# Optimization experiments

Measured on AMD Instinct MI355X. Metric: run time of the kernel, lower is better.

The kernel has to match this reference:

```python
import jax, jax.numpy as jnp
import numpy as np

N_NODES = 100000


def _lightgcn_layer(x, src, dst, norm):
    # message: norm * x[src]; aggregate: mean over incoming edges at dst
    msg = norm[:, None] * x[src]                                   # [E+N, D]
    s = jax.ops.segment_sum(msg, dst, num_segments=N_NODES)        # [N, D]
    cnt = jax.ops.segment_sum(jnp.ones_like(norm), dst, num_segments=N_NODES)
    return s / cnt[:, None]                                        # deg>=1 due to self-loops


def _graph_embeddings(emb, edge_index):
    n = emb.shape[0]
    loop = jnp.arange(n, dtype=edge_index.dtype)
    src = jnp.concatenate([edge_index[0], loop])                   # self-loops appended
    dst = jnp.concatenate([edge_index[1], loop])
    deg = jax.ops.segment_sum(jnp.ones(src.shape[0], emb.dtype), src, num_segments=N_NODES)
    dis = deg ** -0.5
    norm = dis[src] * dis[dst]
    x = emb
    acc = emb
    for _ in range(2):  # num_layers
        x = _lightgcn_layer(x, src, dst, norm)
        acc = acc + x
    return acc / 3.0  # mean over (num_layers + 1) embeddings


def setup_inputs() -> dict:
    key = jax.random.key(0)
    k1, k2, k3, k4 = jax.random.split(key, 4)
    emb = jax.random.normal(k1, (N_NODES, 128), dtype=jnp.float32) * 0.02
    edge_index = jax.random.randint(k2, (2, 600000), 0, N_NODES, dtype=jnp.int64)
    items = jax.random.randint(k3, (4096, 1), 0, N_NODES, dtype=jnp.int64)
    samples = jax.random.randint(k4, (4096, 100), 0, N_NODES, dtype=jnp.int64)
    return {"emb": emb, "edge_index": edge_index, "items": items, "samples": samples}


def reference(emb, edge_index, items, samples):
    embeddings = _graph_embeddings(emb, edge_index)                # [N, D]
    item_emb = embeddings[items]                                   # [B, 1, D]
    sample_emb = embeddings[samples]                               # [B, S, D]
    scores = jnp.einsum('bod,bsd->bos', item_emb, sample_emb)      # [B, 1, S]
    return scores.squeeze(1)                                       # [B, S]
```

## Files before the change

### kernel.cpp

```cpp
#include <hip/hip_runtime.h>

#define NN 100000
#define D 128
#define W 32
#define EPT 2
#define HRS 50000
#define HWORDS 25000
#define HSPLIT 64

__device__ __forceinline__ unsigned short f2bf(float f) {
    unsigned u = __float_as_uint(f);
    u += 0x7FFF + ((u >> 16) & 1);
    return (unsigned short)(u >> 16);
}
__device__ __forceinline__ float bflo(unsigned u) { return __uint_as_float(u << 16); }
__device__ __forceinline__ float bfhi(unsigned u) { return __uint_as_float(u & 0xFFFF0000u); }
__device__ __forceinline__ unsigned pack2(float a, float b) {
    return (unsigned)f2bf(a) | ((unsigned)f2bf(b) << 16);
}
__device__ __forceinline__ void addrow(float* acc, const uint4 v, float w) {
    acc[0] += w * bflo(v.x); acc[1] += w * bfhi(v.x);
    acc[2] += w * bflo(v.y); acc[3] += w * bfhi(v.y);
    acc[4] += w * bflo(v.z); acc[5] += w * bfhi(v.z);
    acc[6] += w * bflo(v.w); acc[7] += w * bfhi(v.w);
}

__global__ __launch_bounds__(256) void hist1_kernel(const int* __restrict__ src,
                                                    unsigned* __restrict__ part,
                                                    int* __restrict__ fillc, int E) {
    __shared__ unsigned h[HWORDS];
    {
        const int per = (NN + 2 * HSPLIT - 1) / (2 * HSPLIT);
        int z0 = blockIdx.x * per;
        int z1 = min(z0 + per, NN);
        for (int t = z0 + (int)threadIdx.x; t < z1; t += 256) fillc[t] = 0;
    }
    int r = blockIdx.x >> 6, c = blockIdx.x & (HSPLIT - 1);
    for (int t = threadIdx.x; t < HWORDS; t += 256) h[t] = 0;
    __syncthreads();
    int chunk = (E + HSPLIT - 1) / HSPLIT;
    int e0 = c * chunk, e1 = min(e0 + chunk, E);
    int lo = r * HRS;
    for (int e = e0 + (int)threadIdx.x; e < e1; e += 256) {
        unsigned s = (unsigned)(src[e] - lo);
        if (s < (unsigned)HRS) atomicAdd(&h[s >> 1], 1u << ((s & 1u) << 4));
    }
    __syncthreads();
    unsigned* dstp = part + (size_t)c * (2 * HWORDS) + (size_t)r * HWORDS;
    for (int t = threadIdx.x; t < HWORDS; t += 256) dstp[t] = h[t];
}

__global__ __launch_bounds__(256) void histB_kernel(const unsigned* __restrict__ part,
                                                    int* __restrict__ deg, int nw) {
    int w = blockIdx.x * 256 + threadIdx.x;
    if (w >= nw) return;
    unsigned s = 0;
    #pragma unroll
    for (int c = 0; c < HSPLIT; ++c) s += part[(size_t)c * (2 * HWORDS) + w];
    deg[2 * w] = (int)(s & 0xFFFFu);
    deg[2 * w + 1] = (int)(s >> 16);
}

__global__ __launch_bounds__(256) void hetero_kernel(const int* __restrict__ src,
                                                     const int* __restrict__ dst,
                                                     const float* __restrict__ emb,
                                                     int* __restrict__ fillc,
                                                     int* __restrict__ ell,
                                                     unsigned short* __restrict__ y0h,
                                                     int E, int EB, int total, int total8) {
    int b = blockIdx.x;
    int lo = (int)(((long long)b * EB) / total);
    int hi = (int)(((long long)(b + 1) * EB) / total);
    if (hi > lo) {
        int e0 = lo * (256 * EPT) + threadIdx.x;
        int e1 = e0 + 256;
        int sa = -1, sb = -1, da = 0, db = 0;
        if (e0 < E) { sa = src[e0]; da = dst[e0]; }
        if (e1 < E) { sb = src[e1]; db = dst[e1]; }
        int pa = -1, pb = -1;
        if (sa >= 0) pa = atomicAdd(&fillc[da], 1);
        if (sb >= 0) pb = atomicAdd(&fillc[db], 1);
        if (sa >= 0 && pa < W) ell[(size_t)da * W + pa] = sa;
        if (sb >= 0 && pb < W) ell[(size_t)db * W + pb] = sb;
    } else {
        int t = (b - hi) * 256 + threadIdx.x;
        if (t < total8) {
            const float4 a = ((const float4*)emb)[t * 2];
            const float4 c = ((const float4*)emb)[t * 2 + 1];
            uint4 o;
            o.x = pack2(a.x, a.y);
            o.y = pack2(a.z, a.w);
            o.z = pack2(c.x, c.y);
            o.w = pack2(c.z, c.w);
            ((uint4*)y0h)[t] = o;
        }
    }
}

__global__ __launch_bounds__(256) void gather1_kernel(const int* __restrict__ ell,
                                                      const int* __restrict__ fillc,
                                                      const int* __restrict__ deg,
                                                      const unsigned short* __restrict__ y0h,
                                                      unsigned short* __restrict__ y1h, int n) {
    unsigned t = blockIdx.x * 256u + threadIdx.x;
    unsigned i = t >> 4, q = t & 15u;
    if (i >= (unsigned)n) return;
    int len = fillc[i];
    int lenc = len > W ? W : len;
    const int* base = ell + (size_t)i * W;
    float wd = rsqrtf((float)deg[i] + 1.0f);
    const uint4 ph = *(const uint4*)(y0h + (size_t)i * D + q * 8);
    float acc[8] = {0.f, 0.f, 0.f, 0.f, 0.f, 0.f, 0.f, 0.f};
    addrow(acc, ph, wd);
    int j = 0;
    for (; j + 4 <= lenc; j += 4) {
        const int4 ss = *(const int4*)(base + j);
        float w0 = rsqrtf((float)deg[ss.x] + 1.0f);
        float w1 = rsqrtf((float)deg[ss.y] + 1.0f);
        float w2 = rsqrtf((float)deg[ss.z] + 1.0f);
        float w3 = rsqrtf((float)deg[ss.w] + 1.0f);
        const uint4 v0 = *(const uint4*)(y0h + (size_t)ss.x * D + q * 8);
        const uint4 v1 = *(const uint4*)(y0h + (size_t)ss.y * D + q * 8);
        const uint4 v2 = *(const uint4*)(y0h + (size_t)ss.z * D + q * 8);
        const uint4 v3 = *(const uint4*)(y0h + (size_t)ss.w * D + q * 8);
        addrow(acc, v0, w0);
        addrow(acc, v1, w1);
        addrow(acc, v2, w2);
        addrow(acc, v3, w3);
    }
    for (; j < lenc; ++j) {
        int s0 = base[j];
        float w0 = rsqrtf((float)deg[s0] + 1.0f);
        const uint4 v0 = *(const uint4*)(y0h + (size_t)s0 * D + q * 8);
        addrow(acc, v0, w0);
    }
    float ci = 1.0f / (float)(len + 1);
    float f1 = ci * wd * wd;
    uint4 o;
    o.x = pack2(f1 * acc[0], f1 * acc[1]);
    o.y = pack2(f1 * acc[2], f1 * acc[3]);
    o.z = pack2(f1 * acc[4], f1 * acc[5]);
    o.w = pack2(f1 * acc[6], f1 * acc[7]);
    *(uint4*)(y1h + (size_t)i * D + q * 8) = o;
}

__global__ __launch_bounds__(256) void gather2_kernel(const int* __restrict__ ell,
                                                      const int* __restrict__ fillc,
                                                      const int* __restrict__ deg,
                                                      const unsigned short* __restrict__ y1h,
                                                      const unsigned short* __restrict__ y0h,
                                                      unsigned short* __restrict__ finh, int n) {
    unsigned t = blockIdx.x * 256u + threadIdx.x;
    unsigned i = t >> 4, q = t & 15u;
    if (i >= (unsigned)n) return;
    int len = fillc[i];
    int lenc = len > W ? W : len;
    const int* base = ell + (size_t)i * W;
    const uint4 ph = *(const uint4*)(y1h + (size_t)i * D + q * 8);
    const uint4 pe = *(const uint4*)(y0h + (size_t)i * D + q * 8);
    float self[8];
    self[0] = bflo(ph.x); self[1] = bfhi(ph.x);
    self[2] = bflo(ph.y); self[3] = bfhi(ph.y);
    self[4] = bflo(ph.z); self[5] = bfhi(ph.z);
    self[6] = bflo(ph.w); self[7] = bfhi(ph.w);
    float acc[8];
    #pragma unroll
    for (int k = 0; k < 8; ++k) acc[k] = self[k];
    int j = 0;
    for (; j + 4 <= lenc; j += 4) {
        const int4 ss = *(const int4*)(base + j);
        const uint4 v0 = *(const uint4*)(y1h + (size_t)ss.x * D + q * 8);
        const uint4 v1 = *(const uint4*)(y1h + (size_t)ss.y * D + q * 8);
        const uint4 v2 = *(const uint4*)(y1h + (size_t)ss.z * D + q * 8);
        const uint4 v3 = *(const uint4*)(y1h + (size_t)ss.w * D + q * 8);
        addrow(acc, v0, 1.0f);
        addrow(acc, v1, 1.0f);
        addrow(acc, v2, 1.0f);
        addrow(acc, v3, 1.0f);
    }
    for (; j < lenc; ++j) {
        int s0 = base[j];
        const uint4 v0 = *(const uint4*)(y1h + (size_t)s0 * D + q * 8);
        addrow(acc, v0, 1.0f);
    }
    float dp1 = (float)deg[i] + 1.0f;
    float wd = rsqrtf(dp1);
    float wdi = sqrtf(dp1);
    float ci = 1.0f / (float)(len + 1);
    float g = ci * wd;
    const float k3 = 1.0f / 3.0f;
    float e[8];
    e[0] = bflo(pe.x); e[1] = bfhi(pe.x);
    e[2] = bflo(pe.y); e[3] = bfhi(pe.y);
    e[4] = bflo(pe.z); e[5] = bfhi(pe.z);
    e[6] = bflo(pe.w); e[7] = bfhi(pe.w);
    float r[8];
    #pragma unroll
    for (int k = 0; k < 8; ++k) r[k] = (e[k] + self[k] * wdi + g * acc[k]) * k3;
    uint4 o;
    o.x = pack2(r[0], r[1]);
    o.y = pack2(r[2], r[3]);
    o.z = pack2(r[4], r[5]);
    o.w = pack2(r[6], r[7]);
    *(uint4*)(finh + (size_t)i * D + q * 8) = o;
}

__global__ __launch_bounds__(256) void scores_kernel(const unsigned short* __restrict__ finh,
                                                     const int* __restrict__ items,
                                                     const int* __restrict__ samples,
                                                     float* __restrict__ out, int S) {
    __shared__ float it[D];
    int b = blockIdx.x;
    if (threadIdx.x < 64) {
        unsigned u = ((const unsigned*)(finh + (size_t)items[b] * D))[threadIdx.x];
        it[threadIdx.x * 2] = bflo(u);
        it[threadIdx.x * 2 + 1] = bfhi(u);
    }
    __syncthreads();
    int g = threadIdx.x >> 4, lane = threadIdx.x & 15;
    float w[8];
    #pragma unroll
    for (int k = 0; k < 8; ++k) w[k] = it[lane * 8 + k];
    int s = g;
    for (; s + 16 < S; s += 32) {
        int node0 = samples[b * S + s];
        int node1 = samples[b * S + s + 16];
        const uint4 v0 = *(const uint4*)(finh + (size_t)node0 * D + lane * 8);
        const uint4 v1 = *(const uint4*)(finh + (size_t)node1 * D + lane * 8);
        float a0 = w[0] * bflo(v0.x) + w[1] * bfhi(v0.x) + w[2] * bflo(v0.y) + w[3] * bfhi(v0.y)
                 + w[4] * bflo(v0.z) + w[5] * bfhi(v0.z) + w[6] * bflo(v0.w) + w[7] * bfhi(v0.w);
        float a1 = w[0] * bflo(v1.x) + w[1] * bfhi(v1.x) + w[2] * bflo(v1.y) + w[3] * bfhi(v1.y)
                 + w[4] * bflo(v1.z) + w[5] * bfhi(v1.z) + w[6] * bflo(v1.w) + w[7] * bfhi(v1.w);
        #pragma unroll
        for (int o = 8; o; o >>= 1) {
            a0 += __shfl_xor(a0, o);
            a1 += __shfl_xor(a1, o);
        }
        if (lane == 0) {
            out[b * S + s] = a0;
            out[b * S + s + 16] = a1;
        }
    }
    if (s < S) {
        int node = samples[b * S + s];
        const uint4 v = *(const uint4*)(finh + (size_t)node * D + lane * 8);
        float a = w[0] * bflo(v.x) + w[1] * bfhi(v.x) + w[2] * bflo(v.y) + w[3] * bfhi(v.y)
                + w[4] * bflo(v.z) + w[5] * bfhi(v.z) + w[6] * bflo(v.w) + w[7] * bfhi(v.w);
        #pragma unroll
        for (int o = 8; o; o >>= 1) a += __shfl_xor(a, o);
        if (lane == 0) out[b * S + s] = a;
    }
}

extern "C" void kernel_launch(void* const* d_in, const int* in_sizes, int n_in,
                              void* d_out, int out_size, void* d_ws, size_t ws_size,
                              hipStream_t stream) {
    const float* emb = (const float*)d_in[0];
    const int* ei = (const int*)d_in[1];
    const int* items = (const int*)d_in[2];
    const int* samples = (const int*)d_in[3];
    float* out = (float*)d_out;

    const int E = in_sizes[1] / 2;
    const int B = in_sizes[2];
    const int S = in_sizes[3] / B;
    const int* src = ei;
    const int* dst = ei + E;

    int* deg = (int*)d_ws;
    int* fillc = deg + NN;
    int* ell = fillc + NN;
    unsigned* part = (unsigned*)(ell + (size_t)NN * W);
    unsigned short* y0h = (unsigned short*)(part + (size_t)HSPLIT * 2 * HWORDS);
    unsigned short* y1h = y0h + (size_t)NN * D;
    unsigned short* finh = y1h + (size_t)NN * D;

    hist1_kernel<<<2 * HSPLIT, 256, 0, stream>>>(src, part, fillc, E);

    const int EB = (E + 256 * EPT - 1) / (256 * EPT);
    const int total8 = NN * D / 8;
    const int CB = (total8 + 255) / 256;
    const int total = EB + CB;
    hetero_kernel<<<total, 256, 0, stream>>>(src, dst, emb, fillc, ell, y0h,
                                             E, EB, total, total8);

    histB_kernel<<<(2 * HWORDS + 255) / 256, 256, 0, stream>>>(part, deg, 2 * HWORDS);

    const int gblocks = (NN * 16 + 255) / 256;
    gather1_kernel<<<gblocks, 256, 0, stream>>>(ell, fillc, deg, y0h, y1h, NN);
    gather2_kernel<<<gblocks, 256, 0, stream>>>(ell, fillc, deg, y1h, y0h, finh, NN);

    scores_kernel<<<B, 256, 0, stream>>>(finh, items, samples, out, S);
}
```

Baseline: 146.4 us.

## Sort nodes by in-degree bucket to balance gather wavefronts

Adds a three-kernel counting sort (per-block histogram, single-block scan, scatter) that builds a permutation of nodes grouped by clamped neighbor count. Both gather kernels then process nodes in this permuted order so lanes in a wavefront have similar loop trip counts, reducing divergence and tail imbalance. This costs three extra small launches and an indirection through perm, and it breaks the contiguous node ordering of the self-row loads and output writes.

```diff
diff --git a/kernel.cpp b/kernel.cpp
--- a/kernel.cpp
+++ b/kernel.cpp
@@ -7,6 +7,11 @@
 #define HRS 50000
 #define HWORDS 25000
 #define HSPLIT 64
+#define LB 98
+#define NPB 1024
+#define NBINS 33
+#define SCTOT (NBINS * LB)
+#define SCPER 13
 
 __device__ __forceinline__ unsigned short f2bf(float f) {
     unsigned u = __float_as_uint(f);
@@ -97,14 +102,79 @@
     }
 }
 
+__global__ __launch_bounds__(256) void lenhistA_kernel(const int* __restrict__ fillc,
+                                                       int* __restrict__ bcnt, int n) {
+    __shared__ int h[NBINS];
+    int b = blockIdx.x;
+    if (threadIdx.x < NBINS) h[threadIdx.x] = 0;
+    __syncthreads();
+    int i0 = b * NPB, i1 = min(i0 + NPB, n);
+    for (int i = i0 + (int)threadIdx.x; i < i1; i += 256) {
+        int len = fillc[i]; if (len > 32) len = 32;
+        atomicAdd(&h[len], 1);
+    }
+    __syncthreads();
+    if (threadIdx.x < NBINS) bcnt[threadIdx.x * LB + b] = h[threadIdx.x];
+}
+
+__global__ __launch_bounds__(256) void lenscan_kernel(const int* __restrict__ bcnt,
+                                                      int* __restrict__ boff) {
+    __shared__ int ws[4];
+    int t = threadIdx.x;
+    int loc[SCPER];
+    int s = 0;
+    int base = t * SCPER;
+    #pragma unroll
+    for (int k = 0; k < SCPER; ++k) {
+        int idx = base + k;
+        int v = (idx < SCTOT) ? bcnt[idx] : 0;
+        loc[k] = s;
+        s += v;
+    }
+    int lane = t & 63, w = t >> 6;
+    int v = s;
+    #pragma unroll
+    for (int o = 1; o < 64; o <<= 1) { int y = __shfl_up(v, o); if (lane >= o) v += y; }
+    if (lane == 63) ws[w] = v;
+    __syncthreads();
+    int add = 0;
+    for (int k = 0; k < w; ++k) add += ws[k];
+    int excl = v + add - s;
+    #pragma unroll
+    for (int k = 0; k < SCPER; ++k) {
+        int idx = base + k;
+        if (idx < SCTOT) boff[idx] = excl + loc[k];
+    }
+}
+
+__global__ __launch_bounds__(256) void lenscat_kernel(const int* __restrict__ fillc,
+                                                      const int* __restrict__ boff,
+                                                      int* __restrict__ perm, int n) {
+    __shared__ int basev[NBINS], cnt[NBINS];
+    int b = blockIdx.x;
+    if (threadIdx.x < NBINS) {
+        basev[threadIdx.x] = boff[threadIdx.x * LB + b];
+        cnt[threadIdx.x] = 0;
+    }
+    __syncthreads();
+    int i0 = b * NPB, i1 = min(i0 + NPB, n);
+    for (int i = i0 + (int)threadIdx.x; i < i1; i += 256) {
+        int len = fillc[i]; if (len > 32) len = 32;
+        int r = atomicAdd(&cnt[len], 1);
+        perm[basev[len] + r] = i;
+    }
+}
+
 __global__ __launch_bounds__(256) void gather1_kernel(const int* __restrict__ ell,
                                                       const int* __restrict__ fillc,
                                                       const int* __restrict__ deg,
+                                                      const int* __restrict__ perm,
                                                       const unsigned short* __restrict__ y0h,
                                                       unsigned short* __restrict__ y1h, int n) {
     unsigned t = blockIdx.x * 256u + threadIdx.x;
-    unsigned i = t >> 4, q = t & 15u;
-    if (i >= (unsigned)n) return;
+    unsigned g = t >> 4, q = t & 15u;
+    if (g >= (unsigned)n) return;
+    unsigned i = (unsigned)perm[g];
     int len = fillc[i];
     int lenc = len > W ? W : len;
     const int* base = ell + (size_t)i * W;
@@ -147,12 +217,14 @@
 __global__ __launch_bounds__(256) void gather2_kernel(const int* __restrict__ ell,
                                                       const int* __restrict__ fillc,
                                                       const int* __restrict__ deg,
+                                                      const int* __restrict__ perm,
                                                       const unsigned short* __restrict__ y1h,
                                                       const unsigned short* __restrict__ y0h,
                                                       unsigned short* __restrict__ finh, int n) {
     unsigned t = blockIdx.x * 256u + threadIdx.x;
-    unsigned i = t >> 4, q = t & 15u;
-    if (i >= (unsigned)n) return;
+    unsigned g = t >> 4, q = t & 15u;
+    if (g >= (unsigned)n) return;
+    unsigned i = (unsigned)perm[g];
     int len = fillc[i];
     int lenc = len > W ? W : len;
     const int* base = ell + (size_t)i * W;
@@ -187,7 +259,7 @@
     float wd = rsqrtf(dp1);
     float wdi = sqrtf(dp1);
     float ci = 1.0f / (float)(len + 1);
-    float g = ci * wd;
+    float g2 = ci * wd;
     const float k3 = 1.0f / 3.0f;
     float e[8];
     e[0] = bflo(pe.x); e[1] = bfhi(pe.x);
@@ -196,7 +268,7 @@
     e[6] = bflo(pe.w); e[7] = bfhi(pe.w);
     float r[8];
     #pragma unroll
-    for (int k = 0; k < 8; ++k) r[k] = (e[k] + self[k] * wdi + g * acc[k]) * k3;
+    for (int k = 0; k < 8; ++k) r[k] = (e[k] + self[k] * wdi + g2 * acc[k]) * k3;
     uint4 o;
     o.x = pack2(r[0], r[1]);
     o.y = pack2(r[2], r[3]);
@@ -271,7 +343,10 @@
     int* fillc = deg + NN;
     int* ell = fillc + NN;
     unsigned* part = (unsigned*)(ell + (size_t)NN * W);
-    unsigned short* y0h = (unsigned short*)(part + (size_t)HSPLIT * 2 * HWORDS);
+    int* bcnt = (int*)(part + (size_t)HSPLIT * 2 * HWORDS);
+    int* boff = bcnt + SCTOT;
+    int* perm = boff + SCTOT;
+    unsigned short* y0h = (unsigned short*)(perm + NN);
     unsigned short* y1h = y0h + (size_t)NN * D;
     unsigned short* finh = y1h + (size_t)NN * D;
 
@@ -286,9 +361,13 @@
 
     histB_kernel<<<(2 * HWORDS + 255) / 256, 256, 0, stream>>>(part, deg, 2 * HWORDS);
 
+    lenhistA_kernel<<<LB, 256, 0, stream>>>(fillc, bcnt, NN);
+    lenscan_kernel<<<1, 256, 0, stream>>>(bcnt, boff);
+    lenscat_kernel<<<LB, 256, 0, stream>>>(fillc, boff, perm, NN);
+
     const int gblocks = (NN * 16 + 255) / 256;
-    gather1_kernel<<<gblocks, 256, 0, stream>>>(ell, fillc, deg, y0h, y1h, NN);
-    gather2_kernel<<<gblocks, 256, 0, stream>>>(ell, fillc, deg, y1h, y0h, finh, NN);
+    gather1_kernel<<<gblocks, 256, 0, stream>>>(ell, fillc, deg, perm, y0h, y1h, NN);
+    gather2_kernel<<<gblocks, 256, 0, stream>>>(ell, fillc, deg, perm, y1h, y0h, finh, NN);
 
     scores_kernel<<<B, 256, 0, stream>>>(finh, items, samples, out, S);
 }
```

Result: slower. 185.1 us (+26.4%).
